# Optimization experiments

Hardware: AMD Instinct MI355X
Metric: run time of the kernel (lower is better)

## Reference

```python
import jax, jax.numpy as jnp
import numpy as np

B, L, D, H = 32, 512, 512, 8


def setup_inputs() -> dict:
    key = jax.random.key(0)
    ks = jax.random.split(key, 6)
    s = 0.02
    return {
        "queries": jax.random.normal(ks[0], (B, L, D), jnp.float32),
        "keys": jax.random.normal(ks[1], (B, L, D), jnp.float32),
        "Wq": jax.random.normal(ks[2], (D, D), jnp.float32) * s,
        "bq": jnp.zeros((D,), jnp.float32),
        "Wk": jax.random.normal(ks[3], (D, D), jnp.float32) * s,
        "bk": jnp.zeros((D,), jnp.float32),
        "Wv": jax.random.normal(ks[4], (D, D), jnp.float32) * s,
        "bv": jnp.zeros((D,), jnp.float32),
        "causality": 1,
    }


def reference(queries, keys, Wq, bq, Wk, bk, Wv, bv, causality):
    b, lq, d = queries.shape
    lk = keys.shape[1]
    dh = d // H

    # torch Linear: x @ W.T + b
    Q = queries @ Wq.T + bq
    K = keys @ Wk.T + bk
    V = keys @ Wv.T + bv

    # chunk along feature dim then cat along batch == head-major [H, B, L, dh]
    def split_heads(x, l):
        return x.reshape(b, l, H, dh).transpose(2, 0, 1, 3)

    Qh = split_heads(Q, lq)
    Kh = split_heads(K, lk)
    Vh = split_heads(V, lk)

    scores = jnp.einsum('hbqd,hbkd->hbqk', Qh, Kh) / jnp.sqrt(jnp.asarray(dh, queries.dtype))

    # sign-based key padding mask: zero rows of `keys` get -inf scores
    key_mask = jnp.sign(jnp.sum(jnp.abs(keys), axis=-1))  # [B, Lk]
    scores = jnp.where(key_mask[None, :, None, :] == 0, -jnp.inf, scores)

    if causality:
        tril = jnp.tril(jnp.ones((lq, lk), dtype=bool))
        scores = jnp.where(tril[None, None, :, :], scores, -jnp.inf)

    w = jax.nn.softmax(scores, axis=-1)
    w = jnp.nan_to_num(w, nan=0.0, posinf=0.0, neginf=0.0)

    # sign-based query mask multiplied AFTER softmax
    query_mask = jnp.sign(jnp.sum(jnp.abs(queries), axis=-1))  # [B, Lq]
    w = w * query_mask[None, :, :, None]

    attention_weights = w.transpose(1, 0, 2, 3)  # [B, H, Lq, Lk]

    # dropout is identity in eval mode
    out = jnp.einsum('hbqk,hbkd->hbqd', w, Vh)          # [H, B, Lq, dh]
    out = out.transpose(1, 2, 0, 3).reshape(b, lq, d)    # head-major concat on feature dim
    return out, attention_weights
```

## Files before the change

kernel.cpp:

```cpp
#include <hip/hip_runtime.h>
#include <math.h>

typedef short short8 __attribute__((ext_vector_type(8)));
typedef short short4v __attribute__((ext_vector_type(4)));
typedef float float4v __attribute__((ext_vector_type(4)));

__device__ __forceinline__ short f2bf(float f) {
    union { float f; unsigned u; } v; v.f = f;
    unsigned r = (v.u + 0x7FFFu + ((v.u >> 16) & 1u)) >> 16;
    return (short)r;
}

__device__ __forceinline__ void async16(const short* g, short* l) {
    __builtin_amdgcn_global_load_lds(
        (const __attribute__((address_space(1))) unsigned*)g,
        (__attribute__((address_space(3))) unsigned*)l, 16, 0, 0);
}

__global__ void cvt_kernel(const float* __restrict__ src, short* __restrict__ dst, int n4) {
    int i = blockIdx.x * blockDim.x + threadIdx.x;
    if (i < n4) {
        float4v v = ((const float4v*)src)[i];
        short4v o;
        o[0] = f2bf(v[0]); o[1] = f2bf(v[1]); o[2] = f2bf(v[2]); o[3] = f2bf(v[3]);
        ((short4v*)dst)[i] = o;
    }
}

__global__ __launch_bounds__(256) void cvtmask_kernel(
    const float* __restrict__ q, const float* __restrict__ k,
    short* __restrict__ qb, short* __restrict__ kb,
    float* __restrict__ qm, float* __restrict__ km) {
    int tid = threadIdx.x;
    int lane = tid & 63, wv = tid >> 6;
    int row = blockIdx.x * 4 + wv;
    const float* src; short* dst; float* msk; int r;
    if (row < 16384) { src = q; dst = qb; msk = qm; r = row; }
    else             { src = k; dst = kb; msk = km; r = row - 16384; }
    const float4v* p = (const float4v*)(src + (size_t)r * 512);
    float4v a = p[lane];
    float4v b = p[lane + 64];
    short4v o1, o2;
    o1[0] = f2bf(a[0]); o1[1] = f2bf(a[1]); o1[2] = f2bf(a[2]); o1[3] = f2bf(a[3]);
    o2[0] = f2bf(b[0]); o2[1] = f2bf(b[1]); o2[2] = f2bf(b[2]); o2[3] = f2bf(b[3]);
    short4v* d4 = (short4v*)(dst + (size_t)r * 512);
    d4[lane] = o1;
    d4[lane + 64] = o2;
    float s = fabsf(a[0]) + fabsf(a[1]) + fabsf(a[2]) + fabsf(a[3])
            + fabsf(b[0]) + fabsf(b[1]) + fabsf(b[2]) + fabsf(b[3]);
    #pragma unroll
    for (int off = 1; off < 64; off <<= 1) s += __shfl_xor(s, off, 64);
    if (lane == 0) msk[r] = (s > 0.f) ? 1.f : 0.f;
}

__global__ __launch_bounds__(256) void proj_kernel(
    const short* __restrict__ Xq, const short* __restrict__ Xk,
    const short* __restrict__ Wqp, const short* __restrict__ Wkp, const short* __restrict__ Wvp,
    const float* __restrict__ bqp, const float* __restrict__ bkp, const float* __restrict__ bvp,
    short* __restrict__ Qo, short* __restrict__ Ko, short* __restrict__ Vo) {
    __shared__ short As[128 * 64];
    __shared__ short Bs[128 * 64];
    int z = blockIdx.z;
    const short* X    = (z == 0) ? Xq  : Xk;
    const short* W    = (z == 0) ? Wqp : (z == 1) ? Wkp : Wvp;
    const float* bias = (z == 0) ? bqp : (z == 1) ? bkp : bvp;
    short* out        = (z == 0) ? Qo  : (z == 1) ? Ko  : Vo;

    int tid = threadIdx.x;
    int lane = tid & 63, wv = tid >> 6;
    int col = lane & 15, quad = lane >> 4;
    int m0 = blockIdx.x * 128;
    int n0 = blockIdx.y * 128;
    int msub = (wv & 1) * 64, nsub = (wv >> 1) * 64;

    float4v acc[4][4];
    #pragma unroll
    for (int mt = 0; mt < 4; ++mt)
        #pragma unroll
        for (int nt = 0; nt < 4; ++nt) { acc[mt][nt][0]=0.f; acc[mt][nt][1]=0.f; acc[mt][nt][2]=0.f; acc[mt][nt][3]=0.f; }

    int rowS = tid >> 3;
    int seg  = tid & 7;
    const short* gA = X + (size_t)(m0 + rowS) * 512 + seg * 8;
    const short* gB = W + (size_t)(n0 + rowS) * 512 + seg * 8;
    short* lA = As + (size_t)tid * 8;
    short* lB = Bs + (size_t)tid * 8;

    for (int k0 = 0; k0 < 512; k0 += 64) {
        __syncthreads();
        #pragma unroll
        for (int j = 0; j < 4; ++j) {
            async16(gA + (size_t)(j * 32) * 512 + k0, lA + j * 2048);
            async16(gB + (size_t)(j * 32) * 512 + k0, lB + j * 2048);
        }
        __syncthreads();
        #pragma unroll
        for (int ksub = 0; ksub < 2; ++ksub) {
            short8 a[4], b[4];
            #pragma unroll
            for (int mt = 0; mt < 4; ++mt)
                a[mt] = *(const short8*)(As + (msub + mt * 16 + col) * 64 + ksub * 32 + quad * 8);
            #pragma unroll
            for (int nt = 0; nt < 4; ++nt)
                b[nt] = *(const short8*)(Bs + (nsub + nt * 16 + col) * 64 + ksub * 32 + quad * 8);
            #pragma unroll
            for (int mt = 0; mt < 4; ++mt)
                #pragma unroll
                for (int nt = 0; nt < 4; ++nt)
                    acc[mt][nt] = __builtin_amdgcn_mfma_f32_16x16x32_bf16(a[mt], b[nt], acc[mt][nt], 0, 0, 0);
        }
    }

    #pragma unroll
    for (int nt = 0; nt < 4; ++nt) {
        float bv = bias[n0 + nsub + nt * 16 + col];
        #pragma unroll
        for (int mt = 0; mt < 4; ++mt) {
            #pragma unroll
            for (int r = 0; r < 4; ++r) {
                int m = m0 + msub + mt * 16 + quad * 4 + r;
                out[(size_t)m * 512 + n0 + nsub + nt * 16 + col] = f2bf(acc[mt][nt][r] + bv);
            }
        }
    }
}

__global__ __launch_bounds__(256) void attn_kernel(
    const short* __restrict__ Q, const short* __restrict__ K, const short* __restrict__ V,
    const float* __restrict__ qmask, const float* __restrict__ kmask,
    const int* __restrict__ caus, float* __restrict__ out, float* __restrict__ aw) {
    __shared__ short vt[64 * 72];
    __shared__ short wl[4 * 16 * 72];

    int tid = threadIdx.x;
    int lane = tid & 63, wv = tid >> 6;
    int col = lane & 15, quad = lane >> 4;
    int bh = blockIdx.x, qt = blockIdx.y;
    int b = bh >> 3, h = bh & 7;
    int q0 = qt * 64 + wv * 16;
    size_t rowbase = (size_t)b * 512;
    bool causal = (*caus) != 0;

    short8 bQ0, bQ1;
    {
        const short* qp = Q + (rowbase + q0 + col) * 512 + h * 64 + quad * 8;
        bQ0 = *(const short8*)(qp);
        bQ1 = *(const short8*)(qp + 32);
    }

    float4v sc[32];
    const short* kp = K + (rowbase + col) * 512 + h * 64 + quad * 8;
    const float* kmp = kmask + b * 512;
    int qg = q0 + col;
    #pragma unroll
    for (int t = 0; t < 32; ++t) {
        short8 aK0 = *(const short8*)(kp + (size_t)(t * 16) * 512);
        short8 aK1 = *(const short8*)(kp + (size_t)(t * 16) * 512 + 32);
        float4v s; s[0]=0.f; s[1]=0.f; s[2]=0.f; s[3]=0.f;
        s = __builtin_amdgcn_mfma_f32_16x16x32_bf16(aK0, bQ0, s, 0, 0, 0);
        s = __builtin_amdgcn_mfma_f32_16x16x32_bf16(aK1, bQ1, s, 0, 0, 0);
        int kb = t * 16 + quad * 4;
        float4v km4 = *(const float4v*)(kmp + kb);
        #pragma unroll
        for (int r = 0; r < 4; ++r) {
            float v = s[r] * 0.125f;
            bool masked = (km4[r] == 0.f) || (causal && (kb + r > qg));
            sc[t][r] = masked ? -INFINITY : v;
        }
    }

    float mx = -INFINITY;
    #pragma unroll
    for (int t = 0; t < 32; ++t)
        #pragma unroll
        for (int r = 0; r < 4; ++r) mx = fmaxf(mx, sc[t][r]);
    mx = fmaxf(mx, __shfl_xor(mx, 16, 64));
    mx = fmaxf(mx, __shfl_xor(mx, 32, 64));
    float sm = 0.f;
    #pragma unroll
    for (int t = 0; t < 32; ++t)
        #pragma unroll
        for (int r = 0; r < 4; ++r) {
            float s = sc[t][r];
            float e = (s == -INFINITY) ? 0.f : __expf(s - mx);
            sc[t][r] = e;
            sm += e;
        }
    sm += __shfl_xor(sm, 16, 64);
    sm += __shfl_xor(sm, 32, 64);
    float qmv = qmask[b * 512 + qg];
    float inv = (sm > 0.f) ? (qmv / sm) : 0.f;
    #pragma unroll
    for (int t = 0; t < 32; ++t)
        #pragma unroll
        for (int r = 0; r < 4; ++r) sc[t][r] *= inv;

    {
        float* awr = aw + ((size_t)b * 8 + h) * 512 * 512 + (size_t)qg * 512 + quad * 4;
        #pragma unroll
        for (int t = 0; t < 32; ++t)
            *(float4v*)(awr + t * 16) = sc[t];
    }

    float4v O[4];
    #pragma unroll
    for (int nt = 0; nt < 4; ++nt) { O[nt][0]=0.f; O[nt][1]=0.f; O[nt][2]=0.f; O[nt][3]=0.f; }
    short* wlw = wl + wv * (16 * 72);
    #pragma unroll
    for (int c = 0; c < 8; ++c) {
        __syncthreads();
        #pragma unroll
        for (int i = 0; i < 2; ++i) {
            int idx = i * 256 + tid;
            int kk = idx >> 3, sg = idx & 7;
            short8 v8 = *(const short8*)(V + (rowbase + c * 64 + kk) * 512 + h * 64 + sg * 8);
            #pragma unroll
            for (int j = 0; j < 8; ++j)
                vt[(sg * 8 + j) * 72 + kk] = v8[j];
        }
        #pragma unroll
        for (int tl = 0; tl < 4; ++tl) {
            int t = c * 4 + tl;
            short4v w4;
            #pragma unroll
            for (int r = 0; r < 4; ++r) w4[r] = f2bf(sc[t][r]);
            *(short4v*)(wlw + col * 72 + tl * 16 + quad * 4) = w4;
        }
        __syncthreads();
        #pragma unroll
        for (int sub = 0; sub < 2; ++sub) {
            short8 aW = *(const short8*)(wlw + col * 72 + sub * 32 + quad * 8);
            #pragma unroll
            for (int nt = 0; nt < 4; ++nt) {
                short8 bV = *(const short8*)(vt + (nt * 16 + col) * 72 + sub * 32 + quad * 8);
                O[nt] = __builtin_amdgcn_mfma_f32_16x16x32_bf16(aW, bV, O[nt], 0, 0, 0);
            }
        }
    }
    #pragma unroll
    for (int nt = 0; nt < 4; ++nt) {
        #pragma unroll
        for (int r = 0; r < 4; ++r) {
            int qq = q0 + quad * 4 + r;
            out[(rowbase + qq) * 512 + h * 64 + nt * 16 + col] = O[nt][r];
        }
    }
}

extern "C" void kernel_launch(void* const* d_in, const int* in_sizes, int n_in,
                              void* d_out, int out_size, void* d_ws, size_t ws_size,
                              hipStream_t stream) {
    const float* queries = (const float*)d_in[0];
    const float* keys    = (const float*)d_in[1];
    const float* Wq      = (const float*)d_in[2];
    const float* bq      = (const float*)d_in[3];
    const float* Wk      = (const float*)d_in[4];
    const float* bk      = (const float*)d_in[5];
    const float* Wv      = (const float*)d_in[6];
    const float* bv      = (const float*)d_in[7];
    const int*   caus    = (const int*)d_in[8];

    const size_t NE = (size_t)16384 * 512;
    short* qbf = (short*)d_ws;
    short* kbf = qbf + NE;
    short* Qb  = kbf + NE;
    short* Kb  = Qb + NE;
    short* Vb  = Kb + NE;
    short* wqb = Vb + NE;
    short* wkb = wqb + 512 * 512;
    short* wvb = wkb + 512 * 512;
    float* qm  = (float*)(wvb + 512 * 512);
    float* km  = qm + 32 * 512;

    cvtmask_kernel<<<8192, 256, 0, stream>>>(queries, keys, qbf, kbf, qm, km);
    cvt_kernel<<<256, 256, 0, stream>>>(Wq, wqb, 65536);
    cvt_kernel<<<256, 256, 0, stream>>>(Wk, wkb, 65536);
    cvt_kernel<<<256, 256, 0, stream>>>(Wv, wvb, 65536);
    dim3 pg(128, 4, 3);
    proj_kernel<<<pg, 256, 0, stream>>>(qbf, kbf, wqb, wkb, wvb, bq, bk, bv, Qb, Kb, Vb);
    float* outp = (float*)d_out;
    float* awp  = outp + 8388608;
    dim3 ag(256, 8);
    attn_kernel<<<ag, 256, 0, stream>>>(Qb, Kb, Vb, qm, km, caus, outp, awp);
}
```

Measured before the change: 513.1 us.

## Skip causally masked tiles and stage all of V once in swizzled LDS

Under causality, the attention kernel now skips QK^T MFMAs, softmax math and PV tiles that lie entirely above the diagonal, and writes zeros straight to the weights output for those tiles. V for the whole head is transposed into a larger XOR-swizzled LDS buffer once, behind a single barrier, replacing the per-chunk load and two syncs. Weight and output stores become nontemporal. The bigger LDS footprint (about 66KB) may reduce blocks per CU. Per-wave loops now have data-dependent bounds, which could cause divergence or extra register pressure.

```diff
diff --git a/kernel.cpp b/kernel.cpp
--- a/kernel.cpp
+++ b/kernel.cpp
@@ -129,7 +129,7 @@
     const short* __restrict__ Q, const short* __restrict__ K, const short* __restrict__ V,
     const float* __restrict__ qmask, const float* __restrict__ kmask,
     const int* __restrict__ caus, float* __restrict__ out, float* __restrict__ aw) {
-    __shared__ short vt[64 * 72];
+    __shared__ short vt[64 * 520];
     __shared__ short wl[4 * 16 * 72];
 
     int tid = threadIdx.x;
@@ -140,6 +140,8 @@
     int q0 = qt * 64 + wv * 16;
     size_t rowbase = (size_t)b * 512;
     bool causal = (*caus) != 0;
+    int lim = causal ? (qt * 4 + wv) : 31;
+    int climit = causal ? qt : 7;
 
     short8 bQ0, bQ1;
     {
@@ -154,53 +156,82 @@
     int qg = q0 + col;
     #pragma unroll
     for (int t = 0; t < 32; ++t) {
-        short8 aK0 = *(const short8*)(kp + (size_t)(t * 16) * 512);
-        short8 aK1 = *(const short8*)(kp + (size_t)(t * 16) * 512 + 32);
-        float4v s; s[0]=0.f; s[1]=0.f; s[2]=0.f; s[3]=0.f;
-        s = __builtin_amdgcn_mfma_f32_16x16x32_bf16(aK0, bQ0, s, 0, 0, 0);
-        s = __builtin_amdgcn_mfma_f32_16x16x32_bf16(aK1, bQ1, s, 0, 0, 0);
-        int kb = t * 16 + quad * 4;
-        float4v km4 = *(const float4v*)(kmp + kb);
-        #pragma unroll
-        for (int r = 0; r < 4; ++r) {
-            float v = s[r] * 0.125f;
-            bool masked = (km4[r] == 0.f) || (causal && (kb + r > qg));
-            sc[t][r] = masked ? -INFINITY : v;
+        if (t <= lim) {
+            short8 aK0 = *(const short8*)(kp + (size_t)(t * 16) * 512);
+            short8 aK1 = *(const short8*)(kp + (size_t)(t * 16) * 512 + 32);
+            float4v s; s[0]=0.f; s[1]=0.f; s[2]=0.f; s[3]=0.f;
+            s = __builtin_amdgcn_mfma_f32_16x16x32_bf16(aK0, bQ0, s, 0, 0, 0);
+            s = __builtin_amdgcn_mfma_f32_16x16x32_bf16(aK1, bQ1, s, 0, 0, 0);
+            int kb = t * 16 + quad * 4;
+            float4v km4 = *(const float4v*)(kmp + kb);
+            #pragma unroll
+            for (int r = 0; r < 4; ++r) {
+                float v = s[r] * 0.125f;
+                bool masked = (km4[r] == 0.f) || (causal && (kb + r > qg));
+                sc[t][r] = masked ? -INFINITY : v;
+            }
+        } else {
+            sc[t][0]=0.f; sc[t][1]=0.f; sc[t][2]=0.f; sc[t][3]=0.f;
         }
     }
 
     float mx = -INFINITY;
     #pragma unroll
     for (int t = 0; t < 32; ++t)
-        #pragma unroll
-        for (int r = 0; r < 4; ++r) mx = fmaxf(mx, sc[t][r]);
+        if (t <= lim) {
+            #pragma unroll
+            for (int r = 0; r < 4; ++r) mx = fmaxf(mx, sc[t][r]);
+        }
     mx = fmaxf(mx, __shfl_xor(mx, 16, 64));
     mx = fmaxf(mx, __shfl_xor(mx, 32, 64));
     float sm = 0.f;
     #pragma unroll
     for (int t = 0; t < 32; ++t)
-        #pragma unroll
-        for (int r = 0; r < 4; ++r) {
-            float s = sc[t][r];
-            float e = (s == -INFINITY) ? 0.f : __expf(s - mx);
-            sc[t][r] = e;
-            sm += e;
+        if (t <= lim) {
+            #pragma unroll
+            for (int r = 0; r < 4; ++r) {
+                float s = sc[t][r];
+                float e = (s == -INFINITY) ? 0.f : __expf(s - mx);
+                sc[t][r] = e;
+                sm += e;
+            }
         }
     sm += __shfl_xor(sm, 16, 64);
     sm += __shfl_xor(sm, 32, 64);
     float qmv = qmask[b * 512 + qg];
     float inv = (sm > 0.f) ? (qmv / sm) : 0.f;
-    #pragma unroll
-    for (int t = 0; t < 32; ++t)
-        #pragma unroll
-        for (int r = 0; r < 4; ++r) sc[t][r] *= inv;
 
     {
         float* awr = aw + ((size_t)b * 8 + h) * 512 * 512 + (size_t)qg * 512 + quad * 4;
-        #pragma unroll
-        for (int t = 0; t < 32; ++t)
-            *(float4v*)(awr + t * 16) = sc[t];
-    }
+        float4v z4; z4[0]=0.f; z4[1]=0.f; z4[2]=0.f; z4[3]=0.f;
+        #pragma unroll
+        for (int t = 0; t < 32; ++t) {
+            if (t <= lim) {
+                #pragma unroll
+                for (int r = 0; r < 4; ++r) sc[t][r] *= inv;
+                __builtin_nontemporal_store(sc[t], (float4v*)(awr + t * 16));
+            } else {
+                __builtin_nontemporal_store(z4, (float4v*)(awr + t * 16));
+            }
+        }
+    }
+
+    #pragma unroll
+    for (int c = 0; c < 8; ++c) {
+        if (c <= climit) {
+            #pragma unroll
+            for (int i = 0; i < 2; ++i) {
+                int idx = i * 256 + tid;
+                int kk = idx >> 3, sg = idx & 7;
+                short8 v8 = *(const short8*)(V + (rowbase + c * 64 + kk) * 512 + h * 64 + sg * 8);
+                int ck = (c * 64 + kk) ^ (sg << 3);
+                #pragma unroll
+                for (int j = 0; j < 8; ++j)
+                    vt[(sg * 8 + j) * 520 + ck] = v8[j];
+            }
+        }
+    }
+    __syncthreads();
 
     float4v O[4];
     #pragma unroll
@@ -208,32 +239,25 @@
     short* wlw = wl + wv * (16 * 72);
     #pragma unroll
     for (int c = 0; c < 8; ++c) {
-        __syncthreads();
-        #pragma unroll
-        for (int i = 0; i < 2; ++i) {
-            int idx = i * 256 + tid;
-            int kk = idx >> 3, sg = idx & 7;
-            short8 v8 = *(const short8*)(V + (rowbase + c * 64 + kk) * 512 + h * 64 + sg * 8);
-            #pragma unroll
-            for (int j = 0; j < 8; ++j)
-                vt[(sg * 8 + j) * 72 + kk] = v8[j];
-        }
-        #pragma unroll
-        for (int tl = 0; tl < 4; ++tl) {
-            int t = c * 4 + tl;
-            short4v w4;
-            #pragma unroll
-            for (int r = 0; r < 4; ++r) w4[r] = f2bf(sc[t][r]);
-            *(short4v*)(wlw + col * 72 + tl * 16 + quad * 4) = w4;
-        }
-        __syncthreads();
-        #pragma unroll
-        for (int sub = 0; sub < 2; ++sub) {
-            short8 aW = *(const short8*)(wlw + col * 72 + sub * 32 + quad * 8);
-            #pragma unroll
-            for (int nt = 0; nt < 4; ++nt) {
-                short8 bV = *(const short8*)(vt + (nt * 16 + col) * 72 + sub * 32 + quad * 8);
-                O[nt] = __builtin_amdgcn_mfma_f32_16x16x32_bf16(aW, bV, O[nt], 0, 0, 0);
+        if (c <= climit) {
+            #pragma unroll
+            for (int tl = 0; tl < 4; ++tl) {
+                int t = c * 4 + tl;
+                short4v w4;
+                #pragma unroll
+                for (int r = 0; r < 4; ++r) w4[r] = f2bf(sc[t][r]);
+                *(short4v*)(wlw + col * 72 + tl * 16 + quad * 4) = w4;
+            }
+            #pragma unroll
+            for (int sub = 0; sub < 2; ++sub) {
+                short8 aW = *(const short8*)(wlw + col * 72 + sub * 32 + quad * 8);
+                #pragma unroll
+                for (int nt = 0; nt < 4; ++nt) {
+                    int d = nt * 16 + col;
+                    int cb = (c * 64 + sub * 32 + quad * 8) ^ (((d >> 3) & 7) << 3);
+                    short8 bV = *(const short8*)(vt + d * 520 + cb);
+                    O[nt] = __builtin_amdgcn_mfma_f32_16x16x32_bf16(aW, bV, O[nt], 0, 0, 0);
+                }
             }
         }
     }
@@ -242,7 +266,8 @@
         #pragma unroll
         for (int r = 0; r < 4; ++r) {
             int qq = q0 + quad * 4 + r;
-            out[(rowbase + qq) * 512 + h * 64 + nt * 16 + col] = O[nt][r];
+            __builtin_nontemporal_store(O[nt][r],
+                out + (rowbase + qq) * 512 + h * 64 + nt * 16 + col);
         }
     }
 }
```

Result: no change. 516.0 us (+0.6%).
